# Optimization experiments

Hardware: AMD Instinct MI355X
Metric: run time of the kernel (lower is better)

Reference implementation:

```python
import jax, jax.numpy as jnp
import numpy as np

D_MODEL = 1024; D_INNER = 2048; HEADDIM = 64; NHEADS = 32; DSTATE = 128
NGROUPS = 1; DCONV = 4; CHUNK = 256; EPS = 1e-5
D_IN_PROJ = 2 * D_INNER + 2 * NGROUPS * DSTATE + NHEADS
CONV_DIM = D_INNER + 2 * NGROUPS * DSTATE
B_SZ = 2; L_SEQ = 4096


def segsum(x):
    # x: (..., T) -> (..., T, T) lower-triangular segment sums (off-diag = -inf)
    T = x.shape[-1]
    cs = jnp.cumsum(x, axis=-1)
    ss = cs[..., :, None] - cs[..., None, :]
    return jnp.where(jnp.tril(jnp.ones((T, T), bool)), ss, -jnp.inf)


def ssd(x, dt, A, Bm, Cm):
    # Chunked SSD selective scan (Mamba2). x:(b,l,h,p) dt:(b,l,h) A:(h,) Bm,Cm:(b,l,g,n)
    b, l, h, p = x.shape
    c = l // CHUNK
    x = x.reshape(b, c, CHUNK, h, p)
    dt = dt.reshape(b, c, CHUNK, h)
    rep = h // NGROUPS
    Bh = jnp.repeat(Bm.reshape(b, c, CHUNK, NGROUPS, DSTATE), rep, axis=3)
    Ch = jnp.repeat(Cm.reshape(b, c, CHUNK, NGROUPS, DSTATE), rep, axis=3)
    xdt = x * dt[..., None]                       # discretized input dt*x
    Adt = (dt * A).transpose(0, 3, 1, 2)          # (b,h,c,T)
    A_cs = jnp.cumsum(Adt, axis=-1)
    Lmat = jnp.exp(segsum(Adt))                   # (b,h,c,T,T) intra-chunk decays
    Y_diag = jnp.einsum('bcthn,bcshn,bhcts,bcshp->bcthp', Ch, Bh, Lmat, xdt)
    decay_states = jnp.exp(A_cs[..., -1:] - A_cs)  # (b,h,c,T)
    states = jnp.einsum('bcthn,bhct,bcthp->bchpn', Bh, decay_states, xdt)
    A_pad = jnp.pad(A_cs[..., -1], ((0, 0), (0, 0), (1, 0)))  # (b,h,c+1)
    decay_chunk = jnp.exp(segsum(A_pad))          # (b,h,c+1,c+1) inter-chunk recurrence
    states = jnp.concatenate([jnp.zeros_like(states[:, :1]), states], axis=1)
    prev = jnp.einsum('bhzc,bchpn->bzhpn', decay_chunk, states)[:, :-1]
    Y_off = jnp.einsum('bcthn,bchpn,bhct->bcthp', Ch, prev, jnp.exp(A_cs))
    return (Y_diag + Y_off).reshape(b, l, h, p)


def mamba_dir(zxbcdt, conv_w, conv_b, dt_bias, A_log, Dp, norm_w):
    # One direction of mamba_split_conv1d_scan_combined (silu act, gated RMSNorm).
    b, l, _ = zxbcdt.shape
    z = zxbcdt[..., :D_INNER]
    xBC = zxbcdt[..., D_INNER:D_INNER + CONV_DIM]
    dt_raw = zxbcdt[..., D_INNER + CONV_DIM:]
    # causal depthwise conv1d (kernel=DCONV) + silu
    xp = jnp.pad(xBC, ((0, 0), (DCONV - 1, 0), (0, 0)))
    conv = conv_b
    for k in range(DCONV):
        conv = conv + conv_w[:, k] * xp[:, k:k + l, :]
    xBC = jax.nn.silu(conv)
    x = xBC[..., :D_INNER].reshape(b, l, NHEADS, HEADDIM)
    Bm = xBC[..., D_INNER:D_INNER + NGROUPS * DSTATE].reshape(b, l, NGROUPS, DSTATE)
    Cm = xBC[..., D_INNER + NGROUPS * DSTATE:].reshape(b, l, NGROUPS, DSTATE)
    dt = jax.nn.softplus(dt_raw + dt_bias)        # (b,l,h)
    A = -jnp.exp(A_log.astype(jnp.float32))       # (h,)
    y = ssd(x, dt, A, Bm, Cm) + x * Dp[None, None, :, None]  # D skip on raw x
    y = y.reshape(b, l, D_INNER)
    y = y * jax.nn.silu(z)                        # gate BEFORE norm (norm_before_gate=False)
    y = y * jax.lax.rsqrt(jnp.mean(y * y, axis=-1, keepdims=True) + EPS) * norm_w
    return y


def setup_inputs():
    rng = np.random.default_rng(0)
    f32 = lambda a: jnp.asarray(a, jnp.float32)
    # dt_bias init per BiMamba2.__init__
    dt = np.exp(rng.uniform(size=NHEADS) * (np.log(0.1) - np.log(0.001)) + np.log(0.001))
    dt = np.clip(dt, 1e-4, None)
    inv_dt = dt + np.log(-np.expm1(-dt))
    A_log = np.log(rng.uniform(1.0, 16.0, NHEADS))
    return dict(
        u=f32(rng.standard_normal((B_SZ, L_SEQ, D_MODEL))),
        in_proj_w=f32(rng.standard_normal((D_IN_PROJ, D_MODEL)) * 0.02),
        conv_w=f32(rng.standard_normal((CONV_DIM, DCONV)) * 0.2),
        conv_b=f32(np.zeros(CONV_DIM)),
        dt_bias=f32(inv_dt),
        A_log=f32(A_log),
        D=f32(np.ones(NHEADS)),
        norm_w=f32(np.ones(D_INNER)),
        bi_conv_w=f32(rng.standard_normal((CONV_DIM, DCONV)) * 0.2),
        bi_conv_b=f32(np.zeros(CONV_DIM)),
        bi_dt_bias=f32(inv_dt.copy()),
        bi_A_log=f32(A_log.copy()),
        bi_D=f32(np.ones(NHEADS)),
        bi_norm_w=f32(np.ones(D_INNER)),
        out_proj_w=f32(rng.standard_normal((D_MODEL, D_INNER)) * 0.02),
    )


def reference(u, in_proj_w, conv_w, conv_b, dt_bias, A_log, D, norm_w,
              bi_conv_w, bi_conv_b, bi_dt_bias, bi_A_log, bi_D, bi_norm_w, out_proj_w):
    zxbcdt = jnp.einsum('bld,ed->ble', u, in_proj_w)
    fwd = mamba_dir(zxbcdt, conv_w, conv_b, dt_bias, A_log, D, norm_w)
    bwd = mamba_dir(zxbcdt[:, ::-1], bi_conv_w, bi_conv_b, bi_dt_bias, bi_A_log, bi_D, bi_norm_w)
    out = (fwd + bwd[:, ::-1]) * 0.5
    return jnp.einsum('ble,de->bld', out, out_proj_w)
```

## Files before the change

kernel.cpp:

```cpp
#include <hip/hip_runtime.h>

#define LSEQ 4096
#define BSZ 2
#define DMODEL 1024
#define DINNER 2048
#define NHEADS 32
#define HEADDIM 64
#define DSTATE 128
#define CHUNK 256
#define NCHUNK 16
#define CONVDIM 2304
#define DINPROJ 4384
#define NPAD 4480
#define BL (BSZ*LSEQ)

typedef unsigned short u16;
typedef unsigned int u32;
typedef u16 u16x4 __attribute__((ext_vector_type(4)));
typedef u16 u16x8 __attribute__((ext_vector_type(8)));
typedef __bf16 bf16x8 __attribute__((ext_vector_type(8)));
typedef float f32x4 __attribute__((ext_vector_type(4)));

__device__ __forceinline__ u16 f2bf(float f){
  union { float f; u32 u; } v; v.f = f;
  u32 r = v.u + 0x7fffu + ((v.u >> 16) & 1u);
  return (u16)(r >> 16);
}
__device__ __forceinline__ float bf2f(u16 h){
  union { u32 u; float f; } v; v.u = ((u32)h) << 16;
  return v.f;
}
__device__ __forceinline__ u32 pack2(float a, float b){
  return (u32)f2bf(a) | ((u32)f2bf(b) << 16);
}
__device__ __forceinline__ f32x4 mfma16(bf16x8 a, bf16x8 b, f32x4 c){
  return __builtin_amdgcn_mfma_f32_16x16x32_bf16(a, b, c, 0, 0, 0);
}
__device__ __forceinline__ void gload16(const void* g, void* l){
  __builtin_amdgcn_global_load_lds((const __attribute__((address_space(1))) void*)g,
                                   (__attribute__((address_space(3))) void*)l, 16, 0, 0);
}

__global__ void sentinel_kernel(float* out){ out[threadIdx.x] = 123456.0f; }

__global__ void cvt_kernel(const float* __restrict__ in, u16* __restrict__ out,
                           long nin, long nout){
  long i = (long)blockIdx.x*blockDim.x + threadIdx.x;
  long stride = (long)gridDim.x*blockDim.x;
  for (; i < nout; i += stride) out[i] = (i < nin) ? f2bf(in[i]) : (u16)0;
}

template<int BF16OUT>
__global__ __launch_bounds__(256) void gemm_bt(const u16* __restrict__ A, const u16* __restrict__ B,
                                               void* __restrict__ Cv, int K, int ldc)
{
  __shared__ u16 As[128*64];
  __shared__ u16 Bs[128*64];
  const int tid = threadIdx.x, lane = tid & 63;
  const int wave = tid >> 6;
  const int wr = wave >> 1, wc = wave & 1;
  f32x4 acc[4][4];
  #pragma unroll
  for (int i=0;i<4;i++)
    #pragma unroll
    for (int j=0;j<4;j++) acc[i][j] = (f32x4){0.f,0.f,0.f,0.f};

  const u16* Ag = A + (size_t)blockIdx.x * 128 * K;
  const u16* Bg = B + (size_t)blockIdx.y * 128 * K;
  const u16* srcG = ((wave < 2) ? Ag : Bg) + (size_t)((wave & 1) * 64) * K;
  u16* dstL = ((wave < 2) ? As : Bs) + (wave & 1) * 64 * 64;
  const int lrow8 = lane >> 3;
  const int scol  = (lane & 7) ^ (lane >> 3);
  const int r = lane & 15, g = lane >> 4;

  for (int kt = 0; kt < K; kt += 64) {
    __syncthreads();
    #pragma unroll
    for (int i=0;i<8;i++){
      const u16* gp = srcG + (size_t)(i*8 + lrow8)*K + kt + scol*8;
      gload16(gp, dstL + i*512);
    }
    __syncthreads();
    #pragma unroll
    for (int kk=0;kk<2;kk++){
      bf16x8 af[4], bfv[4];
      #pragma unroll
      for (int mt=0;mt<4;mt++)
        af[mt] = *(const bf16x8*)&As[(wr*64+mt*16+r)*64 + (((kk*4+g) ^ (r&7))*8)];
      #pragma unroll
      for (int nt=0;nt<4;nt++)
        bfv[nt] = *(const bf16x8*)&Bs[(wc*64+nt*16+r)*64 + (((kk*4+g) ^ (r&7))*8)];
      #pragma unroll
      for (int mt=0;mt<4;mt++)
        #pragma unroll
        for (int nt=0;nt<4;nt++)
          acc[mt][nt] = mfma16(af[mt], bfv[nt], acc[mt][nt]);
    }
  }
  const size_t cbase = (size_t)(blockIdx.x*128 + wr*64 + g*4) * ldc
                     + blockIdx.y*128 + wc*64 + r;
  if (BF16OUT) {
    u16* Cg = (u16*)Cv + cbase;
    #pragma unroll
    for (int mt=0;mt<4;mt++)
      #pragma unroll
      for (int nt=0;nt<4;nt++)
        #pragma unroll
        for (int j=0;j<4;j++)
          Cg[(size_t)(mt*16+j)*ldc + nt*16] = f2bf(acc[mt][nt][j]);
  } else {
    float* Cg = (float*)Cv + cbase;
    #pragma unroll
    for (int mt=0;mt<4;mt++)
      #pragma unroll
      for (int nt=0;nt<4;nt++)
        #pragma unroll
        for (int j=0;j<4;j++)
          Cg[(size_t)(mt*16+j)*ldc + nt*16] = acc[mt][nt][j];
  }
}

__global__ __launch_bounds__(320) void conv_kernel(
    const u16* __restrict__ zxh, const float* __restrict__ cw, const float* __restrict__ cb,
    const float* __restrict__ dtb,
    u16* __restrict__ xout, u16* __restrict__ Bout, u16* __restrict__ Cout,
    float* __restrict__ dtt, int rev)
{
  const int l = blockIdx.x, b = blockIdx.y, tid = threadIdx.x;
  if (tid < 288){
    const int ch0 = tid*8;
    f32x4 cw4[8];
    #pragma unroll
    for (int j=0;j<8;j++) cw4[j] = *(const f32x4*)&cw[(ch0+j)*4];
    float acc[8];
    {
      f32x4 b0 = *(const f32x4*)&cb[ch0];
      f32x4 b1 = *(const f32x4*)&cb[ch0+4];
      #pragma unroll
      for (int j=0;j<4;j++){ acc[j] = b0[j]; acc[4+j] = b1[j]; }
    }
    #pragma unroll
    for (int k=0;k<4;k++){
      int ls = l - 3 + k;
      if (ls >= 0){
        int lsrc = rev ? (LSEQ-1-ls) : ls;
        u16x8 v = *(const u16x8*)(zxh + ((size_t)b*LSEQ + lsrc)*NPAD + DINNER + ch0);
        #pragma unroll
        for (int j=0;j<8;j++) acc[j] += cw4[j][k] * bf2f(v[j]);
      }
    }
    u16x8 o;
    #pragma unroll
    for (int j=0;j<8;j++){
      float sv = acc[j] / (1.f + __expf(-acc[j]));
      o[j] = f2bf(sv);
    }
    if (ch0 < DINNER)
      *(u16x8*)(xout + ((size_t)b*LSEQ + l)*DINNER + ch0) = o;
    else if (ch0 < DINNER+DSTATE)
      *(u16x8*)(Bout + ((size_t)b*LSEQ + l)*DSTATE + (ch0 - DINNER)) = o;
    else
      *(u16x8*)(Cout + ((size_t)b*LSEQ + l)*DSTATE + (ch0 - DINNER - DSTATE)) = o;
  } else {
    const int hh = tid - 288;
    const int lsrc = rev ? (LSEQ-1-l) : l;
    float raw = bf2f(zxh[((size_t)b*LSEQ + lsrc)*NPAD + DINNER + CONVDIM + hh]) + dtb[hh];
    float dv = (raw > 20.f) ? raw : log1pf(__expf(raw));
    dtt[((size_t)b*NHEADS + hh)*LSEQ + l] = dv;
  }
}

__global__ __launch_bounds__(256) void acs_kernel(const float* __restrict__ dtt,
    const float* __restrict__ A_log, float* __restrict__ acs)
{
  const int c = blockIdx.x, hh = blockIdx.y, b = blockIdx.z;
  const int t = threadIdx.x;
  __shared__ float s[CHUNK];
  const float Ah = -__expf(A_log[hh]);
  const size_t base = ((size_t)b*NHEADS + hh)*LSEQ + (size_t)c*CHUNK;
  s[t] = dtt[base + t] * Ah;
  __syncthreads();
  for (int off=1; off<CHUNK; off<<=1){
    float add = (t >= off) ? s[t-off] : 0.f;
    __syncthreads();
    s[t] += add;
    __syncthreads();
  }
  acs[base + t] = s[t];
}

__global__ __launch_bounds__(256) void states_kernel(
    const u16* __restrict__ xb, const u16* __restrict__ Bb,
    const float* __restrict__ dtt, const float* __restrict__ acs,
    u16* __restrict__ states)
{
  const int h = blockIdx.x, c = blockIdx.y, b = blockIdx.z;
  const int tid = threadIdx.x, lane = tid & 63, w = tid >> 6;
  __shared__ float acs_s[CHUNK], dt_s[CHUNK];
  __shared__ u32 xdtTW[64*20];
  __shared__ u32 BsdW[128*20];

  const size_t bhBase = ((size_t)b*NHEADS + h)*LSEQ + (size_t)c*CHUNK;
  acs_s[tid] = acs[bhBase + tid];
  dt_s[tid]  = dtt[bhBase + tid];
  __syncthreads();
  const float acsLast = acs_s[CHUNK-1];

  f32x4 sacc[4][2];
  #pragma unroll
  for (int i=0;i<4;i++){ sacc[i][0] = (f32x4){0,0,0,0}; sacc[i][1] = (f32x4){0,0,0,0}; }

  const int s2 = tid >> 4, q = tid & 15;
  const int g = lane >> 4, r = lane & 15;
  const size_t rowBase = (size_t)b*LSEQ + (size_t)c*CHUNK;
  for (int st8 = 0; st8 < 8; ++st8) {
    const int s0 = st8*32;
    const int sA = s0 + 2*s2, sB = sA + 1;
    u16x4 xA = *(const u16x4*)(xb + (rowBase+sA)*DINNER + h*HEADDIM + 4*q);
    u16x4 xB4 = *(const u16x4*)(xb + (rowBase+sB)*DINNER + h*HEADDIM + 4*q);
    u16x8 bA = *(const u16x8*)(Bb + (rowBase+sA)*DSTATE + 8*q);
    u16x8 bB = *(const u16x8*)(Bb + (rowBase+sB)*DSTATE + 8*q);
    const float dA = dt_s[sA], dB = dt_s[sB];
    const float eA = __expf(acsLast - acs_s[sA]), eB = __expf(acsLast - acs_s[sB]);
    __syncthreads();
    #pragma unroll
    for (int j=0;j<4;j++){
      int p = 4*q + j;
      xdtTW[p*20 + (s2 ^ (((p>>3)&3)<<2))] = pack2(bf2f(xA[j])*dA, bf2f(xB4[j])*dB);
    }
    #pragma unroll
    for (int j=0;j<8;j++){
      int n = 8*q + j;
      BsdW[n*20 + (s2 ^ (((n>>3)&3)<<2))] = pack2(bf2f(bA[j])*eA, bf2f(bB[j])*eB);
    }
    __syncthreads();
    bf16x8 xf[4];
    #pragma unroll
    for (int pt=0;pt<4;pt++){
      int p = pt*16 + r;
      xf[pt] = *(const bf16x8*)&xdtTW[p*20 + 4*(g ^ ((p>>3)&3))];
    }
    #pragma unroll
    for (int nt=0;nt<2;nt++){
      int n = w*32 + nt*16 + r;
      bf16x8 bdf = *(const bf16x8*)&BsdW[n*20 + 4*(g ^ ((n>>3)&3))];
      #pragma unroll
      for (int pt=0;pt<4;pt++) sacc[pt][nt] = mfma16(xf[pt], bdf, sacc[pt][nt]);
    }
  }
  u16* sp = states + (((size_t)b*NCHUNK + c)*NHEADS + h)*(size_t)(HEADDIM*DSTATE);
  #pragma unroll
  for (int pt=0;pt<4;pt++)
    #pragma unroll
    for (int nt=0;nt<2;nt++)
      #pragma unroll
      for (int j=0;j<4;j++)
        sp[(size_t)(pt*16+g*4+j)*DSTATE + w*32+nt*16+r] = f2bf(sacc[pt][nt][j]);
}

__global__ __launch_bounds__(256) void recur_kernel(const u16* __restrict__ states,
    const float* __restrict__ acs, u16* __restrict__ prev)
{
  const int bx = blockIdx.x;
  const int seg = bx & 7, bh = bx >> 3;
  const int b = bh >> 5, h = bh & 31;
  const int tid = threadIdx.x;
  float S[4];
  #pragma unroll
  for (int k=0;k<4;k++) S[k] = 0.f;
  for (int c=0;c<NCHUNK;c++){
    const size_t off = (((size_t)b*NCHUNK + c)*NHEADS + h)*(size_t)(HEADDIM*DSTATE)
                     + seg*1024;
    const float dc = __expf(acs[((size_t)b*NHEADS+h)*LSEQ + (size_t)c*CHUNK + CHUNK-1]);
    #pragma unroll
    for (int k=0;k<4;k++){
      const size_t i = off + tid + k*256;
      prev[i] = f2bf(S[k]);
      S[k] = S[k]*dc + bf2f(states[i]);
    }
  }
}

__global__ __launch_bounds__(256) void ydiagoff_kernel(
    const u16* __restrict__ xb, const u16* __restrict__ Bb, const u16* __restrict__ Cb,
    const float* __restrict__ dtt, const float* __restrict__ acs,
    const u16* __restrict__ prev, const float* __restrict__ Dp,
    u16* __restrict__ ydir)
{
  const int h = blockIdx.x, c = blockIdx.y, b = blockIdx.z;
  const int tid = threadIdx.x, lane = tid & 63, w = tid >> 6;
  __shared__ float acs_s[CHUNK], dt_s[CHUNK];
  __shared__ u16 Bs[32][136];
  __shared__ u32 xdtTW[64*20];
  __shared__ u16 Ms[4][64][40];

  const size_t bhBase = ((size_t)b*NHEADS + h)*LSEQ + (size_t)c*CHUNK;
  acs_s[tid] = acs[bhBase + tid];
  dt_s[tid]  = dtt[bhBase + tid];
  __syncthreads();

  const int g = lane >> 4, r = lane & 15;
  const size_t rowBase = (size_t)b*LSEQ + (size_t)c*CHUNK;

  bf16x8 caf[4][4];
  const u16* Crow = Cb + rowBase*DSTATE;
  #pragma unroll
  for (int mt=0;mt<4;mt++)
    #pragma unroll
    for (int ks=0;ks<4;ks++)
      caf[mt][ks] = *(const bf16x8*)(Crow + (size_t)(mt*64+w*16+r)*DSTATE + ks*32 + g*8);

  f32x4 yacc[4][4];
  #pragma unroll
  for (int i=0;i<4;i++)
    #pragma unroll
    for (int j=0;j<4;j++) yacc[i][j] = (f32x4){0,0,0,0};

  const int sl = tid >> 3, part = tid & 7;
  const int s2 = tid >> 4, q = tid & 15;
  for (int st8 = 0; st8 < 8; ++st8) {
    const int s0 = st8*32;
    u16x8 v0 = *(const u16x8*)(Bb + (rowBase + s0 + sl)*DSTATE + part*16);
    u16x8 v1 = *(const u16x8*)(Bb + (rowBase + s0 + sl)*DSTATE + part*16 + 8);
    const int sA = s0 + 2*s2, sB = sA + 1;
    u16x4 xA = *(const u16x4*)(xb + (rowBase+sA)*DINNER + h*HEADDIM + 4*q);
    u16x4 xB4 = *(const u16x4*)(xb + (rowBase+sB)*DINNER + h*HEADDIM + 4*q);
    const float dA = dt_s[sA], dB = dt_s[sB];
    __syncthreads();
    *(u16x8*)&Bs[sl][part*16]   = v0;
    *(u16x8*)&Bs[sl][part*16+8] = v1;
    #pragma unroll
    for (int j=0;j<4;j++){
      int p = 4*q + j;
      xdtTW[p*20 + (s2 ^ (((p>>3)&3)<<2))] = pack2(bf2f(xA[j])*dA, bf2f(xB4[j])*dB);
    }
    __syncthreads();
    bf16x8 xf[4];
    #pragma unroll
    for (int pt=0;pt<4;pt++){
      int p = pt*16 + r;
      xf[pt] = *(const bf16x8*)&xdtTW[p*20 + 4*(g ^ ((p>>3)&3))];
    }
    #pragma unroll
    for (int mt=0;mt<4;mt++){
      if (4*mt + w >= 2*st8) {
        f32x4 g20 = (f32x4){0,0,0,0}, g21 = (f32x4){0,0,0,0};
        #pragma unroll
        for (int ks=0;ks<4;ks++){
          bf16x8 bfv0 = *(const bf16x8*)&Bs[r][ks*32+g*8];
          bf16x8 bfv1 = *(const bf16x8*)&Bs[16+r][ks*32+g*8];
          g20 = mfma16(caf[mt][ks], bfv0, g20);
          g21 = mfma16(caf[mt][ks], bfv1, g21);
        }
        #pragma unroll
        for (int j=0;j<4;j++){
          int tl = mt*64 + w*16 + g*4 + j;
          int sg0 = s0 + r;
          int sg1 = s0 + 16 + r;
          float m0 = (sg0 <= tl) ? g20[j]*__expf(acs_s[tl]-acs_s[sg0]) : 0.f;
          float m1 = (sg1 <= tl) ? g21[j]*__expf(acs_s[tl]-acs_s[sg1]) : 0.f;
          Ms[w][mt*16+g*4+j][r]    = f2bf(m0);
          Ms[w][mt*16+g*4+j][16+r] = f2bf(m1);
        }
        bf16x8 mf = *(const bf16x8*)&Ms[w][mt*16+r][g*8];
        #pragma unroll
        for (int pt=0;pt<4;pt++) yacc[mt][pt] = mfma16(mf, xf[pt], yacc[mt][pt]);
      }
    }
  }
  #pragma unroll
  for (int mt=0;mt<4;mt++){
    const float et = __expf(acs_s[mt*64 + w*16 + r]);
    #pragma unroll
    for (int ks=0;ks<4;ks++)
      #pragma unroll
      for (int e=0;e<8;e++)
        caf[mt][ks][e] = (__bf16)((float)caf[mt][ks][e] * et);
  }
  const u16* pv = prev + (((size_t)b*NCHUNK + c)*NHEADS + h)*(size_t)(HEADDIM*DSTATE);
  #pragma unroll
  for (int ks=0;ks<4;ks++){
    bf16x8 pf[4];
    #pragma unroll
    for (int pt=0;pt<4;pt++)
      pf[pt] = *(const bf16x8*)(pv + (size_t)(pt*16+r)*DSTATE + ks*32 + g*8);
    #pragma unroll
    for (int mt=0;mt<4;mt++)
      #pragma unroll
      for (int pt=0;pt<4;pt++) yacc[mt][pt] = mfma16(caf[mt][ks], pf[pt], yacc[mt][pt]);
  }
  const float Dh = Dp[h];
  const u16* xrow = xb + rowBase*DINNER + h*HEADDIM;
  u16* yrow = ydir + rowBase*DINNER + h*HEADDIM;
  #pragma unroll
  for (int mt=0;mt<4;mt++)
    #pragma unroll
    for (int pt=0;pt<4;pt++)
      #pragma unroll
      for (int j=0;j<4;j++){
        int tl = mt*64 + w*16 + g*4 + j;
        int p  = pt*16 + r;
        float xv = bf2f(xrow[(size_t)tl*DINNER + p]);
        yrow[(size_t)tl*DINNER + p] = f2bf(yacc[mt][pt][j] + xv*Dh);
      }
}

__global__ __launch_bounds__(256) void gate_norm_kernel(
    const u16* __restrict__ ydir, const u16* __restrict__ zxh,
    const float* __restrict__ nw, u16* __restrict__ ybufh, int rev)
{
  const int l = blockIdx.x, b = blockIdx.y, tid = threadIdx.x;
  const int lsrc = rev ? (LSEQ-1-l) : l;
  u16x8 zv = *(const u16x8*)(zxh + ((size_t)b*LSEQ + lsrc)*NPAD + tid*8);
  u16x8 yv = *(const u16x8*)(ydir + ((size_t)b*LSEQ + l)*DINNER + tid*8);
  float gg[8]; float ss = 0.f;
  #pragma unroll
  for (int j=0;j<8;j++){
    float z = bf2f(zv[j]);
    float y = bf2f(yv[j]);
    float v = y * (z / (1.f + __expf(-z)));
    gg[j] = v; ss += v*v;
  }
  #pragma unroll
  for (int off=32; off>0; off>>=1) ss += __shfl_xor(ss, off, 64);
  __shared__ float red[4];
  if ((tid&63)==0) red[tid>>6] = ss;
  __syncthreads();
  float tot = red[0]+red[1]+red[2]+red[3];
  float scale = rsqrtf(tot * (1.f/DINNER) + 1e-5f);
  const float* nwp = nw + tid*8;
  u16* hrow = ybufh + ((size_t)b*LSEQ + lsrc)*DINNER + tid*8;
  u16x8 o;
  if (!rev){
    #pragma unroll
    for (int j=0;j<8;j++) o[j] = f2bf(0.5f * gg[j]*scale*nwp[j]);
  } else {
    u16x8 pvv = *(const u16x8*)hrow;
    #pragma unroll
    for (int j=0;j<8;j++) o[j] = f2bf(bf2f(pvv[j]) + 0.5f*gg[j]*scale*nwp[j]);
  }
  *(u16x8*)hrow = o;
}

extern "C" void kernel_launch(void* const* d_in, const int* in_sizes, int n_in,
                              void* d_out, int out_size, void* d_ws, size_t ws_size,
                              hipStream_t stream) {
  const float* u        = (const float*)d_in[0];
  const float* w1       = (const float*)d_in[1];
  const float* conv_w   = (const float*)d_in[2];
  const float* conv_b   = (const float*)d_in[3];
  const float* dt_bias  = (const float*)d_in[4];
  const float* A_log    = (const float*)d_in[5];
  const float* Dp       = (const float*)d_in[6];
  const float* norm_w   = (const float*)d_in[7];
  const float* bconv_w  = (const float*)d_in[8];
  const float* bconv_b  = (const float*)d_in[9];
  const float* bdt_bias = (const float*)d_in[10];
  const float* bA_log   = (const float*)d_in[11];
  const float* bDp      = (const float*)d_in[12];
  const float* bnorm_w  = (const float*)d_in[13];
  const float* wo       = (const float*)d_in[14];
  float* out = (float*)d_out;

  const size_t SZ_ZX  = (size_t)BL*NPAD*2;
  const size_t SZ_UB  = (size_t)BL*DMODEL*2;
  const size_t SZ_W1  = (size_t)NPAD*DMODEL*2;
  const size_t SZ_WO  = (size_t)DMODEL*DINNER*2;
  const size_t SZ_XB  = (size_t)BL*DINNER*2;
  const size_t SZ_BB  = (size_t)BL*DSTATE*2;
  const size_t SZ_DT  = (size_t)BSZ*NHEADS*LSEQ*4;
  const size_t SZ_ST  = (size_t)BSZ*NCHUNK*NHEADS*HEADDIM*DSTATE*2;
  const size_t SZ_YD  = (size_t)BL*DINNER*2;
  const size_t SZ_YH  = (size_t)BL*DINNER*2;
  const size_t NEED = SZ_ZX + SZ_UB + SZ_W1 + SZ_WO + SZ_XB + 2*SZ_BB + 2*SZ_DT
                    + SZ_ST + SZ_YD + SZ_YH;
  if (ws_size < NEED) { sentinel_kernel<<<1,256,0,stream>>>(out); return; }

  char* p = (char*)d_ws;
  u16*   zxh    = (u16*)p;              p += SZ_ZX;
  u16*   ub     = (u16*)p;              p += SZ_UB;
  u16*   states = ub;
  u16*   w1b    = (u16*)p;              p += SZ_W1;
  u16*   wob    = (u16*)p;              p += SZ_WO;
  u16*   xb     = (u16*)p;              p += SZ_XB;
  u16*   Bb     = (u16*)p;              p += SZ_BB;
  u16*   Cb     = (u16*)p;              p += SZ_BB;
  float* dtt    = (float*)p;            p += SZ_DT;
  float* acs    = (float*)p;            p += SZ_DT;
  u16*   prev   = (u16*)p;              p += SZ_ST;
  u16*   ydir   = (u16*)p;              p += SZ_YD;
  u16*   ybufh  = (u16*)p;              p += SZ_YH;

  cvt_kernel<<<2048,256,0,stream>>>(u,  ub,  (long)BL*DMODEL,      (long)BL*DMODEL);
  cvt_kernel<<<2048,256,0,stream>>>(w1, w1b, (long)DINPROJ*DMODEL, (long)NPAD*DMODEL);
  cvt_kernel<<<2048,256,0,stream>>>(wo, wob, (long)DMODEL*DINNER,  (long)DMODEL*DINNER);

  gemm_bt<1><<<dim3(BL/128, NPAD/128),256,0,stream>>>(ub, w1b, zxh, DMODEL, NPAD);

  for (int dir = 0; dir < 2; ++dir) {
    const float* cwp = dir ? bconv_w  : conv_w;
    const float* cbp = dir ? bconv_b  : conv_b;
    const float* dbp = dir ? bdt_bias : dt_bias;
    const float* alp = dir ? bA_log   : A_log;
    const float* ddp = dir ? bDp      : Dp;
    const float* nwp = dir ? bnorm_w  : norm_w;
    conv_kernel<<<dim3(LSEQ,BSZ),320,0,stream>>>(zxh, cwp, cbp, dbp, xb, Bb, Cb, dtt, dir);
    acs_kernel<<<dim3(NCHUNK,NHEADS,BSZ),256,0,stream>>>(dtt, alp, acs);
    states_kernel<<<dim3(NHEADS,NCHUNK,BSZ),256,0,stream>>>(xb, Bb, dtt, acs, states);
    recur_kernel<<<BSZ*NHEADS*8,256,0,stream>>>(states, acs, prev);
    ydiagoff_kernel<<<dim3(NHEADS,NCHUNK,BSZ),256,0,stream>>>(xb, Bb, Cb, dtt, acs, prev, ddp, ydir);
    gate_norm_kernel<<<dim3(LSEQ,BSZ),256,0,stream>>>(ydir, zxh, nwp, ybufh, dir);
  }

  gemm_bt<0><<<dim3(BL/128, DMODEL/128),256,0,stream>>>(ybufh, wob, out, DINNER, DMODEL);
}
```

Baseline: 478.1 us.

## Precompute head-shared C·Bᵀ chunk matrix once instead of per head

```diff
diff --git a/kernel.cpp b/kernel.cpp
--- a/kernel.cpp
+++ b/kernel.cpp
@@ -189,6 +189,45 @@
   acs[base + t] = s[t];
 }
 
+__global__ __launch_bounds__(256) void gmat_kernel(
+    const u16* __restrict__ Bb, const u16* __restrict__ Cb, u16* __restrict__ gbuf)
+{
+  const int c = blockIdx.x, b = blockIdx.y, st8 = blockIdx.z;
+  const int tid = threadIdx.x, lane = tid & 63, w = tid >> 6;
+  __shared__ u16 Bs[32][136];
+  const int g = lane >> 4, r = lane & 15;
+  const size_t rowBase = (size_t)b*LSEQ + (size_t)c*CHUNK;
+  const int s0 = st8*32;
+  const int sl = tid >> 3, part = tid & 7;
+  {
+    u16x8 v0 = *(const u16x8*)(Bb + (rowBase + s0 + sl)*DSTATE + part*16);
+    u16x8 v1 = *(const u16x8*)(Bb + (rowBase + s0 + sl)*DSTATE + part*16 + 8);
+    *(u16x8*)&Bs[sl][part*16]   = v0;
+    *(u16x8*)&Bs[sl][part*16+8] = v1;
+  }
+  __syncthreads();
+  const u16* Crow = Cb + rowBase*DSTATE;
+  #pragma unroll
+  for (int mt=0; mt<4; ++mt){
+    const int ms = 4*mt + w;
+    if (ms < 2*st8) continue;
+    f32x4 g20 = (f32x4){0,0,0,0}, g21 = (f32x4){0,0,0,0};
+    #pragma unroll
+    for (int ks=0;ks<4;ks++){
+      bf16x8 cf = *(const bf16x8*)(Crow + (size_t)(mt*64+w*16+r)*DSTATE + ks*32 + g*8);
+      bf16x8 bfv0 = *(const bf16x8*)&Bs[r][ks*32+g*8];
+      bf16x8 bfv1 = *(const bf16x8*)&Bs[16+r][ks*32+g*8];
+      g20 = mfma16(cf, bfv0, g20);
+      g21 = mfma16(cf, bfv1, g21);
+    }
+    u16x8 ov;
+    #pragma unroll
+    for (int j=0;j<4;j++){ ov[j] = f2bf(g20[j]); ov[4+j] = f2bf(g21[j]); }
+    const size_t idx = ((((size_t)(b*NCHUNK + c)*8 + st8)*16 + ms)*64 + lane)*8;
+    *(u16x8*)(gbuf + idx) = ov;
+  }
+}
+
 __global__ __launch_bounds__(256) void states_kernel(
     const u16* __restrict__ xb, const u16* __restrict__ Bb,
     const float* __restrict__ dtt, const float* __restrict__ acs,
@@ -282,15 +321,14 @@
 }
 
 __global__ __launch_bounds__(256) void ydiagoff_kernel(
-    const u16* __restrict__ xb, const u16* __restrict__ Bb, const u16* __restrict__ Cb,
+    const u16* __restrict__ xb, const u16* __restrict__ Cb,
     const float* __restrict__ dtt, const float* __restrict__ acs,
-    const u16* __restrict__ prev, const float* __restrict__ Dp,
-    u16* __restrict__ ydir)
+    const u16* __restrict__ prev, const u16* __restrict__ gbuf,
+    const float* __restrict__ Dp, u16* __restrict__ ydir)
 {
   const int h = blockIdx.x, c = blockIdx.y, b = blockIdx.z;
   const int tid = threadIdx.x, lane = tid & 63, w = tid >> 6;
   __shared__ float acs_s[CHUNK], dt_s[CHUNK];
-  __shared__ u16 Bs[32][136];
   __shared__ u32 xdtTW[64*20];
   __shared__ u16 Ms[4][64][40];
 
@@ -301,14 +339,7 @@
 
   const int g = lane >> 4, r = lane & 15;
   const size_t rowBase = (size_t)b*LSEQ + (size_t)c*CHUNK;
-
-  bf16x8 caf[4][4];
-  const u16* Crow = Cb + rowBase*DSTATE;
-  #pragma unroll
-  for (int mt=0;mt<4;mt++)
-    #pragma unroll
-    for (int ks=0;ks<4;ks++)
-      caf[mt][ks] = *(const bf16x8*)(Crow + (size_t)(mt*64+w*16+r)*DSTATE + ks*32 + g*8);
+  const size_t gBase = (((size_t)(b*NCHUNK + c))*8)*16*64*8;
 
   f32x4 yacc[4][4];
   #pragma unroll
@@ -316,19 +347,14 @@
     #pragma unroll
     for (int j=0;j<4;j++) yacc[i][j] = (f32x4){0,0,0,0};
 
-  const int sl = tid >> 3, part = tid & 7;
   const int s2 = tid >> 4, q = tid & 15;
   for (int st8 = 0; st8 < 8; ++st8) {
     const int s0 = st8*32;
-    u16x8 v0 = *(const u16x8*)(Bb + (rowBase + s0 + sl)*DSTATE + part*16);
-    u16x8 v1 = *(const u16x8*)(Bb + (rowBase + s0 + sl)*DSTATE + part*16 + 8);
     const int sA = s0 + 2*s2, sB = sA + 1;
     u16x4 xA = *(const u16x4*)(xb + (rowBase+sA)*DINNER + h*HEADDIM + 4*q);
     u16x4 xB4 = *(const u16x4*)(xb + (rowBase+sB)*DINNER + h*HEADDIM + 4*q);
     const float dA = dt_s[sA], dB = dt_s[sB];
     __syncthreads();
-    *(u16x8*)&Bs[sl][part*16]   = v0;
-    *(u16x8*)&Bs[sl][part*16+8] = v1;
     #pragma unroll
     for (int j=0;j<4;j++){
       int p = 4*q + j;
@@ -344,21 +370,15 @@
     #pragma unroll
     for (int mt=0;mt<4;mt++){
       if (4*mt + w >= 2*st8) {
-        f32x4 g20 = (f32x4){0,0,0,0}, g21 = (f32x4){0,0,0,0};
-        #pragma unroll
-        for (int ks=0;ks<4;ks++){
-          bf16x8 bfv0 = *(const bf16x8*)&Bs[r][ks*32+g*8];
-          bf16x8 bfv1 = *(const bf16x8*)&Bs[16+r][ks*32+g*8];
-          g20 = mfma16(caf[mt][ks], bfv0, g20);
-          g21 = mfma16(caf[mt][ks], bfv1, g21);
-        }
+        const size_t idx = gBase + (((size_t)st8*16 + (4*mt+w))*64 + lane)*8;
+        u16x8 gv = *(const u16x8*)(gbuf + idx);
         #pragma unroll
         for (int j=0;j<4;j++){
           int tl = mt*64 + w*16 + g*4 + j;
           int sg0 = s0 + r;
           int sg1 = s0 + 16 + r;
-          float m0 = (sg0 <= tl) ? g20[j]*__expf(acs_s[tl]-acs_s[sg0]) : 0.f;
-          float m1 = (sg1 <= tl) ? g21[j]*__expf(acs_s[tl]-acs_s[sg1]) : 0.f;
+          float m0 = (sg0 <= tl) ? bf2f(gv[j])*__expf(acs_s[tl]-acs_s[sg0]) : 0.f;
+          float m1 = (sg1 <= tl) ? bf2f(gv[4+j])*__expf(acs_s[tl]-acs_s[sg1]) : 0.f;
           Ms[w][mt*16+g*4+j][r]    = f2bf(m0);
           Ms[w][mt*16+g*4+j][16+r] = f2bf(m1);
         }
@@ -368,14 +388,18 @@
       }
     }
   }
+  const u16* Crow = Cb + rowBase*DSTATE;
+  bf16x8 caf[4][4];
   #pragma unroll
   for (int mt=0;mt<4;mt++){
     const float et = __expf(acs_s[mt*64 + w*16 + r]);
     #pragma unroll
-    for (int ks=0;ks<4;ks++)
+    for (int ks=0;ks<4;ks++){
+      caf[mt][ks] = *(const bf16x8*)(Crow + (size_t)(mt*64+w*16+r)*DSTATE + ks*32 + g*8);
       #pragma unroll
       for (int e=0;e<8;e++)
         caf[mt][ks][e] = (__bf16)((float)caf[mt][ks][e] * et);
+    }
   }
   const u16* pv = prev + (((size_t)b*NCHUNK + c)*NHEADS + h)*(size_t)(HEADDIM*DSTATE);
   #pragma unroll
@@ -472,8 +496,9 @@
   const size_t SZ_ST  = (size_t)BSZ*NCHUNK*NHEADS*HEADDIM*DSTATE*2;
   const size_t SZ_YD  = (size_t)BL*DINNER*2;
   const size_t SZ_YH  = (size_t)BL*DINNER*2;
+  const size_t SZ_GB  = (size_t)BSZ*NCHUNK*8*16*64*8*2;
   const size_t NEED = SZ_ZX + SZ_UB + SZ_W1 + SZ_WO + SZ_XB + 2*SZ_BB + 2*SZ_DT
-                    + SZ_ST + SZ_YD + SZ_YH;
+                    + SZ_ST + SZ_YD + SZ_YH + SZ_GB;
   if (ws_size < NEED) { sentinel_kernel<<<1,256,0,stream>>>(out); return; }
 
   char* p = (char*)d_ws;
@@ -490,6 +515,7 @@
   u16*   prev   = (u16*)p;              p += SZ_ST;
   u16*   ydir   = (u16*)p;              p += SZ_YD;
   u16*   ybufh  = (u16*)p;              p += SZ_YH;
+  u16*   gbuf   = (u16*)p;              p += SZ_GB;
 
   cvt_kernel<<<2048,256,0,stream>>>(u,  ub,  (long)BL*DMODEL,      (long)BL*DMODEL);
   cvt_kernel<<<2048,256,0,stream>>>(w1, w1b, (long)DINPROJ*DMODEL, (long)NPAD*DMODEL);
@@ -506,9 +532,10 @@
     const float* nwp = dir ? bnorm_w  : norm_w;
     conv_kernel<<<dim3(LSEQ,BSZ),320,0,stream>>>(zxh, cwp, cbp, dbp, xb, Bb, Cb, dtt, dir);
     acs_kernel<<<dim3(NCHUNK,NHEADS,BSZ),256,0,stream>>>(dtt, alp, acs);
+    gmat_kernel<<<dim3(NCHUNK,BSZ,8),256,0,stream>>>(Bb, Cb, gbuf);
     states_kernel<<<dim3(NHEADS,NCHUNK,BSZ),256,0,stream>>>(xb, Bb, dtt, acs, states);
     recur_kernel<<<BSZ*NHEADS*8,256,0,stream>>>(states, acs, prev);
-    ydiagoff_kernel<<<dim3(NHEADS,NCHUNK,BSZ),256,0,stream>>>(xb, Bb, Cb, dtt, acs, prev, ddp, ydir);
+    ydiagoff_kernel<<<dim3(NHEADS,NCHUNK,BSZ),256,0,stream>>>(xb, Cb, dtt, acs, prev, gbuf, ddp, ydir);
     gate_norm_kernel<<<dim3(LSEQ,BSZ),256,0,stream>>>(ydir, zxh, nwp, ybufh, dir);
   }
 
```

New measurement: 534.5 us. 11.8% more time.
